# Performance work log

Hardware: AMD Instinct MI355X
Metric: run time of the kernel (lower is better)

The kernel has to match this reference:

```python
import jax, jax.numpy as jnp
import numpy as np

B, N, C, H = 8, 1024, 768, 12
HD = C // H  # 64


def setup_inputs() -> dict:
    key = jax.random.key(0)
    k0, k1, k2, k3, k4 = jax.random.split(key, 5)
    x = jax.random.normal(k0, (B, N, C), jnp.float32)
    # ToMe token sizes are counts >= 1; sample in [1, 16)
    size = jax.random.uniform(k1, (B, N, 1), jnp.float32, minval=1.0, maxval=16.0)
    key_padding_mask = jax.random.randint(k2, (B, N), 0, 2).astype(jnp.bool_)
    w_qkv = jax.random.normal(k3, (3 * C, C), jnp.float32) * (C ** -0.5)
    w_proj = jax.random.normal(k4, (C, C), jnp.float32) * (C ** -0.5)
    b_proj = jnp.zeros((C,), jnp.float32)
    return dict(x=x, size=size, key_padding_mask=key_padding_mask,
                w_qkv=w_qkv, w_proj=w_proj, b_proj=b_proj)


def reference(x, size, key_padding_mask, w_qkv, w_proj, b_proj):
    b, n, c = x.shape
    hd = c // H
    scale = hd ** -0.5
    # qkv projection: [B,N,3C] -> [3,B,H,N,hd]
    qkv = (x @ w_qkv.T).reshape(b, n, 3, H, hd).transpose(2, 0, 3, 1, 4)
    q, k, v = qkv[0], qkv[1], qkv[2]
    # raw scores [B,H,N,N]
    attn = jnp.einsum('bhnd,bhmd->bhnm', q, k) * scale
    # proportional attention: additive log-size bias over keys
    attn = attn + jnp.log(size)[:, None, None, :, 0]
    # key padding mask: True -> -inf
    attn = jnp.where(key_padding_mask[:, None, None, :], -jnp.inf, attn)
    attn = jax.nn.softmax(attn, axis=-1)
    # PV, back to [B,N,C]
    out = jnp.einsum('bhnm,bhmd->bnhd', attn, v).reshape(b, n, c)
    out = out @ w_proj.T + b_proj
    # mean of k over heads: [B,N,hd]
    k_mean = k.mean(axis=1)
    return out, k_mean
```

## Files before the change

kernel.cpp:

```cpp
#include <hip/hip_runtime.h>

typedef __bf16 bf16;
typedef __bf16 bf16x4 __attribute__((ext_vector_type(4)));
typedef __bf16 bf16x8 __attribute__((ext_vector_type(8)));
typedef float f32x4 __attribute__((ext_vector_type(4)));

#define MFMA_16x16x32(a, b, c) __builtin_amdgcn_mfma_f32_16x16x32_bf16((a), (b), (c), 0, 0, 0)

#define B_ 8
#define N_ 1024
#define C_ 768
#define H_ 12
#define HD_ 64
#define KDIM 768

__device__ __forceinline__ void gload_lds16(const void* g, void* l) {
  __builtin_amdgcn_global_load_lds(
      (const __attribute__((address_space(1))) void*)g,
      (__attribute__((address_space(3))) void*)l, 16, 0, 0);
}

__global__ __launch_bounds__(256) void detect_mask_kernel(const unsigned* __restrict__ m32,
                                                          int* __restrict__ flags) {
  const int i = blockIdx.x * 256 + threadIdx.x;
  if (i < 2048) {
    const unsigned v = m32[i];
    if (v > 1u) atomicOr(&flags[0], 1);
    if ((i & 1) && v != 0u) atomicOr(&flags[1], 1);
  }
}

__global__ __launch_bounds__(256) void cvt_kernel(const float* __restrict__ x,
                                                  const float* __restrict__ wq,
                                                  const float* __restrict__ wp,
                                                  const float* __restrict__ size_in,
                                                  const void* __restrict__ mask_raw,
                                                  const int* __restrict__ flags,
                                                  bf16* __restrict__ xb,
                                                  bf16* __restrict__ wqb,
                                                  bf16* __restrict__ wpb,
                                                  float* __restrict__ biasb) {
  const int i = blockIdx.x * 256 + threadIdx.x;
  {
    const float4 v = ((const float4*)x)[i];
    bf16x4 o = {(bf16)v.x, (bf16)v.y, (bf16)v.z, (bf16)v.w};
    ((bf16x4*)xb)[i] = o;
  }
  if (i < 442368) {
    const float4 v = ((const float4*)wq)[i];
    bf16x4 o = {(bf16)v.x, (bf16)v.y, (bf16)v.z, (bf16)v.w};
    ((bf16x4*)wqb)[i] = o;
  }
  if (i < 147456) {
    const float4 v = ((const float4*)wp)[i];
    bf16x4 o = {(bf16)v.x, (bf16)v.y, (bf16)v.z, (bf16)v.w};
    ((bf16x4*)wpb)[i] = o;
  }
  if (i < B_ * N_) {
    int mv;
    if (flags[0]) {
      mv = (int)((const unsigned char*)mask_raw)[i];
    } else if (flags[1]) {
      mv = ((const int*)mask_raw)[i];
    } else {
      const unsigned* m32 = (const unsigned*)mask_raw;
      mv = (int)(m32[2 * i] | m32[2 * i + 1]);
    }
    biasb[i] = mv ? -1e30f : logf(size_in[i]);
  }
}

template <int MODE>
__global__ __launch_bounds__(256) void gemm_bt(const bf16* __restrict__ A,
                                               const bf16* __restrict__ W,
                                               const float* __restrict__ bias,
                                               bf16* __restrict__ out0,
                                               bf16* __restrict__ out1,
                                               bf16* __restrict__ out2,
                                               float* __restrict__ outf) {
  __shared__ bf16 As[2][128 * 64];
  __shared__ bf16 Bs[2][128 * 64];
  const int bid = blockIdx.x;
  const int mt = bid % 64;
  const int nt = bid / 64;
  const int t = threadIdx.x;
  const int lane = t & 63, w = t >> 6;
  const int wm = w >> 1, wn = w & 1;
  const int l15 = lane & 15, lg = lane >> 4;

  f32x4 acc[4][4] = {};

  const int srow = t >> 3;
  const int skel = ((t & 7) ^ (srow & 7)) * 8;
  const bf16* Ag = A + (size_t)(mt * 128) * KDIM;
  const bf16* Bg = W + (size_t)(nt * 128) * KDIM;
  const int bA = mt >> 3;
  const int nbase = (mt & 7) * 128;

#define ASRC(st, c)                                                          \
  ((MODE == 0)                                                               \
       ? (Ag + (size_t)((c) * 32 + srow) * KDIM + (st) * 64 + skel)          \
       : (A + (((size_t)(bA * 12 + (st)) * 1024) + nbase + (c) * 32 + srow)  \
              * 64 + skel))
#define BSRC(st, c) (Bg + (size_t)((c) * 32 + srow) * KDIM + (st) * 64 + skel)

#pragma unroll
  for (int c = 0; c < 4; ++c) {
    gload_lds16(ASRC(0, c), (char*)As[0] + c * 4096 + w * 1024);
    gload_lds16(BSRC(0, c), (char*)Bs[0] + c * 4096 + w * 1024);
  }
  __syncthreads();

  const int swz = l15 & 7;

  for (int st = 0; st < KDIM / 64; ++st) {
    const int cur = st & 1;
    if (st < KDIM / 64 - 1) {
#pragma unroll
      for (int c = 0; c < 4; ++c) {
        gload_lds16(ASRC(st + 1, c), (char*)As[cur ^ 1] + c * 4096 + w * 1024);
        gload_lds16(BSRC(st + 1, c), (char*)Bs[cur ^ 1] + c * 4096 + w * 1024);
      }
    }
#pragma unroll
    for (int ks = 0; ks < 2; ++ks) {
      bf16x8 af[4], bfr[4];
#pragma unroll
      for (int i = 0; i < 4; ++i)
        af[i] = *(const bf16x8*)(As[cur] + (wm * 64 + i * 16 + l15) * 64 +
                                 ((ks * 4 + lg) ^ swz) * 8);
#pragma unroll
      for (int i = 0; i < 4; ++i)
        bfr[i] = *(const bf16x8*)(Bs[cur] + (wn * 64 + i * 16 + l15) * 64 +
                                  ((ks * 4 + lg) ^ swz) * 8);
#pragma unroll
      for (int i = 0; i < 4; ++i)
#pragma unroll
        for (int j = 0; j < 4; ++j)
          acc[i][j] = MFMA_16x16x32(af[i], bfr[j], acc[i][j]);
    }
    __syncthreads();
  }
#undef ASRC
#undef BSRC

  if (MODE == 0) {
    const int which = (nt * 128) / 768;
#pragma unroll
    for (int i = 0; i < 4; ++i)
#pragma unroll
      for (int j = 0; j < 4; ++j)
#pragma unroll
        for (int r = 0; r < 4; ++r) {
          const int m = mt * 128 + wm * 64 + i * 16 + lg * 4 + r;
          const int o = nt * 128 + wn * 64 + j * 16 + l15;
          const int b = m >> 10, n = m & 1023;
          const int f = o - which * 768;
          const int h = f >> 6, hd = f & 63;
          const bf16 bv = (bf16)acc[i][j][r];
          if (which == 0)
            out0[(((size_t)(b * 12 + h)) * 1024 + n) * 64 + hd] = bv;
          else if (which == 1)
            out1[(((size_t)(b * 12 + h)) * 1024 + n) * 64 + hd] = bv;
          else
            out2[(((size_t)(b * 12 + h)) * 64 + hd) * 1024 + n] = bv;
        }
  } else {
#pragma unroll
    for (int i = 0; i < 4; ++i)
#pragma unroll
      for (int j = 0; j < 4; ++j) {
        const int o = nt * 128 + wn * 64 + j * 16 + l15;
        const float bv = bias[o];
#pragma unroll
        for (int r = 0; r < 4; ++r) {
          const int m = mt * 128 + wm * 64 + i * 16 + lg * 4 + r;
          outf[(size_t)m * 768 + o] = acc[i][j][r] + bv;
        }
      }
  }
}

__global__ __launch_bounds__(256) void kmean_kernel(const bf16* __restrict__ kbuf,
                                                    float* __restrict__ kmean) {
  const int i = blockIdx.x * 256 + threadIdx.x;
  if (i >= B_ * N_ * HD_) return;
  const int hd = i & 63;
  const int n = (i >> 6) & 1023;
  const int b = i >> 16;
  float s = 0.f;
#pragma unroll
  for (int h = 0; h < 12; ++h)
    s += (float)kbuf[(((size_t)(b * 12 + h)) * 1024 + n) * 64 + hd];
  kmean[i] = s * (1.0f / 12.0f);
}

__global__ __launch_bounds__(512, 4) void attn_mfma(const bf16* __restrict__ qbuf,
                                                    const bf16* __restrict__ kbuf,
                                                    const bf16* __restrict__ vtbuf,
                                                    const float* __restrict__ biasb,
                                                    bf16* __restrict__ outws) {
  __shared__ bf16 Ks[2][4096];
  __shared__ bf16 Vs[2][4096];
  const int id = blockIdx.x;
  const int qt = id & 3;
  const int bh = id >> 2;
  const int b = bh / 12;
  const int t = threadIdx.x, lane = t & 63, w = t >> 6;
  const int l15 = lane & 15, lg = lane >> 4;
  const int qbase = qt * 256 + w * 16;

  const bf16* Q = qbuf + ((size_t)bh * 1024 + qbase) * 64;
  const bf16* Kp = kbuf + (size_t)bh * 65536;
  const bf16* Vt = vtbuf + (size_t)bh * 65536;
  const float* bias = biasb + b * 1024;

  const bf16x8 qb0 = *(const bf16x8*)(Q + l15 * 64 + lg * 8);
  const bf16x8 qb1 = *(const bf16x8*)(Q + l15 * 64 + 32 + lg * 8);
  const bf16x8 qc0 = *(const bf16x8*)(Q + (128 + l15) * 64 + lg * 8);
  const bf16x8 qc1 = *(const bf16x8*)(Q + (128 + l15) * 64 + 32 + lg * 8);

  const int srow = t >> 3;
  const int dsl = (t & 7) ^ (srow & 7);
  const int kkey = 32 * ((srow >> 5) & 1) + 4 * ((srow >> 4) & 1) +
                   8 * ((srow >> 2) & 3) + (srow & 3);
  const bf16* srcK = Kp + kkey * 64 + dsl * 8;
  const bf16* srcV = Vt + (size_t)srow * 1024 + dsl * 8;

  gload_lds16(srcK, (char*)&Ks[0][0] + w * 1024);
  gload_lds16(srcV, (char*)&Vs[0][0] + w * 1024);
  __syncthreads();

  const int bb0 = 8 * lg;
  const int swz = l15 & 7;

  f32x4 oacc[4] = {}, oacc2[4] = {};
  float m = -1e30f, l = 0.f;
  float m2 = -1e30f, l2 = 0.f;

  for (int kt = 0; kt < 16; ++kt) {
    const int cur = kt & 1;
    const int kb = kt * 64;
    if (kt < 15) {
      gload_lds16(srcK + (size_t)(kb + 64) * 64, (char*)&Ks[cur ^ 1][0] + w * 1024);
      gload_lds16(srcV + (kb + 64), (char*)&Vs[cur ^ 1][0] + w * 1024);
    }

    const bf16* LK = Ks[cur];
    const bf16* LV = Vs[cur];
    float sv[4][4], sw[4][4];
#pragma unroll
    for (int f = 0; f < 4; ++f) {
      const int cf = 32 * (f >> 1) + 4 * (f & 1);
      const bf16* kj = LK + (f * 16 + l15) * 64;
      const bf16x8 ka0 = *(const bf16x8*)(kj + (lg ^ swz) * 8);
      const bf16x8 ka1 = *(const bf16x8*)(kj + ((lg + 4) ^ swz) * 8);
      f32x4 z = {}, y = {};
      z = MFMA_16x16x32(ka0, qb0, z);
      y = MFMA_16x16x32(ka0, qc0, y);
      z = MFMA_16x16x32(ka1, qb1, z);
      y = MFMA_16x16x32(ka1, qc1, y);
      const float4 bi = *(const float4*)(bias + kb + cf + bb0);
      sv[f][0] = z[0] * 0.125f + bi.x;
      sv[f][1] = z[1] * 0.125f + bi.y;
      sv[f][2] = z[2] * 0.125f + bi.z;
      sv[f][3] = z[3] * 0.125f + bi.w;
      sw[f][0] = y[0] * 0.125f + bi.x;
      sw[f][1] = y[1] * 0.125f + bi.y;
      sw[f][2] = y[2] * 0.125f + bi.z;
      sw[f][3] = y[3] * 0.125f + bi.w;
    }
    float mx = sv[0][0], mx2 = sw[0][0];
#pragma unroll
    for (int f = 0; f < 4; ++f)
#pragma unroll
      for (int j = 0; j < 4; ++j) {
        mx = fmaxf(mx, sv[f][j]);
        mx2 = fmaxf(mx2, sw[f][j]);
      }
    mx = fmaxf(mx, __shfl_xor(mx, 16, 64));
    mx = fmaxf(mx, __shfl_xor(mx, 32, 64));
    mx2 = fmaxf(mx2, __shfl_xor(mx2, 16, 64));
    mx2 = fmaxf(mx2, __shfl_xor(mx2, 32, 64));
    const float mn = fmaxf(m, mx);
    const float mn2 = fmaxf(m2, mx2);
    const float resc = __expf(m - mn);
    const float resc2 = __expf(m2 - mn2);
    m = mn;
    m2 = mn2;

    float rs = 0.f, rs2 = 0.f;
    bf16x8 pa0, pa1, pa2, pa3;
#pragma unroll
    for (int f = 0; f < 4; ++f)
#pragma unroll
      for (int j = 0; j < 4; ++j) {
        const float p = __expf(sv[f][j] - mn);
        const float p2 = __expf(sw[f][j] - mn2);
        rs += p;
        rs2 += p2;
        const bf16 pb = (bf16)p;
        const bf16 pb2 = (bf16)p2;
        if (f == 0) { pa0[j] = pb; pa2[j] = pb2; }
        else if (f == 1) { pa0[4 + j] = pb; pa2[4 + j] = pb2; }
        else if (f == 2) { pa1[j] = pb; pa3[j] = pb2; }
        else { pa1[4 + j] = pb; pa3[4 + j] = pb2; }
      }
    rs += __shfl_xor(rs, 16, 64);
    rs += __shfl_xor(rs, 32, 64);
    rs2 += __shfl_xor(rs2, 16, 64);
    rs2 += __shfl_xor(rs2, 32, 64);
    l = l * resc + rs;
    l2 = l2 * resc2 + rs2;

#pragma unroll
    for (int df = 0; df < 4; ++df) {
      const bf16* vj = LV + (df * 16 + l15) * 64;
      const bf16x8 va0 = *(const bf16x8*)(vj + (lg ^ swz) * 8);
      const bf16x8 va1 = *(const bf16x8*)(vj + ((lg + 4) ^ swz) * 8);
      f32x4 t4 = oacc[df];
      f32x4 u4 = oacc2[df];
#pragma unroll
      for (int j = 0; j < 4; ++j) {
        t4[j] *= resc;
        u4[j] *= resc2;
      }
      t4 = MFMA_16x16x32(va0, pa0, t4);
      u4 = MFMA_16x16x32(va0, pa2, u4);
      t4 = MFMA_16x16x32(va1, pa1, t4);
      u4 = MFMA_16x16x32(va1, pa3, u4);
      oacc[df] = t4;
      oacc2[df] = u4;
    }
    __syncthreads();
  }

  const float inv = 1.0f / l;
  const float inv2 = 1.0f / l2;
  bf16* outp = outws + ((size_t)bh * 1024 + qbase + l15) * 64;
#pragma unroll
  for (int df = 0; df < 4; ++df) {
    bf16x4 ov = {(bf16)(oacc[df][0] * inv), (bf16)(oacc[df][1] * inv),
                 (bf16)(oacc[df][2] * inv), (bf16)(oacc[df][3] * inv)};
    *(bf16x4*)(outp + df * 16 + lg * 4) = ov;
    bf16x4 ov2 = {(bf16)(oacc2[df][0] * inv2), (bf16)(oacc2[df][1] * inv2),
                  (bf16)(oacc2[df][2] * inv2), (bf16)(oacc2[df][3] * inv2)};
    *(bf16x4*)(outp + (size_t)128 * 64 + df * 16 + lg * 4) = ov2;
  }
}

extern "C" void kernel_launch(void* const* d_in, const int* in_sizes, int n_in,
                              void* d_out, int out_size, void* d_ws, size_t ws_size,
                              hipStream_t stream) {
  const float* x       = (const float*)d_in[0];
  const float* size_in = (const float*)d_in[1];
  const void*  mask    = d_in[2];
  const float* w_qkv   = (const float*)d_in[3];
  const float* w_proj  = (const float*)d_in[4];
  const float* b_proj  = (const float*)d_in[5];
  float* out = (float*)d_out;

  if (n_in < 6 ||
      in_sizes[0] != 6291456 || in_sizes[1] != 8192 || in_sizes[2] != 8192 ||
      in_sizes[3] != 1769472 || in_sizes[4] != 589824 || in_sizes[5] != 768)
    return;

  const size_t QS = (size_t)B_ * H_ * N_ * HD_;
  if (ws_size < 55083024) return;

  bf16* xb    = (bf16*)d_ws;
  bf16* qbuf  = xb + QS;
  bf16* kbuf  = qbuf + QS;
  bf16* vtbuf = kbuf + QS;
  bf16* wqb   = vtbuf + QS;
  bf16* wpb   = wqb + 1769472;
  float* biasb = (float*)(wpb + 589824);
  int* flags = (int*)(biasb + 8192);
  bf16* attnw = xb;

  hipMemsetAsync(flags, 0, 8, stream);
  detect_mask_kernel<<<8, 256, 0, stream>>>((const unsigned*)mask, flags);
  cvt_kernel<<<6144, 256, 0, stream>>>(x, w_qkv, w_proj, size_in, mask, flags,
                                       xb, wqb, wpb, biasb);
  gemm_bt<0><<<64 * 18, 256, 0, stream>>>(xb, wqb, nullptr, qbuf, kbuf, vtbuf, nullptr);
  kmean_kernel<<<2048, 256, 0, stream>>>(kbuf, out + (size_t)B_ * N_ * C_);
  attn_mfma<<<384, 512, 0, stream>>>(qbuf, kbuf, vtbuf, biasb, attnw);
  gemm_bt<1><<<64 * 6, 256, 0, stream>>>(attnw, wpb, b_proj, nullptr, nullptr, nullptr, out);
}
```

Before: 165.5 us.

## Use 256x256 single-buffered tiles with 512 threads for QKV GEMM

Splits the templated GEMM into a dedicated QKV kernel and a projection kernel. The QKV GEMM moves from 128x128 tiles with 256 threads and double-buffered LDS to 256x256 tiles with 8 waves, each wave holding a 128x64 accumulator. The larger tile raises data reuse per LDS load and cuts the grid from 1152 to 288 blocks. In exchange it drops the double buffering, so loads and compute no longer overlap within a block. Register pressure also rises, and 288 blocks may leave some CUs on the 256-CU part underused.

```diff
diff --git a/kernel.cpp b/kernel.cpp
--- a/kernel.cpp
+++ b/kernel.cpp
@@ -70,14 +70,83 @@
   }
 }
 
-template <int MODE>
-__global__ __launch_bounds__(256) void gemm_bt(const bf16* __restrict__ A,
-                                               const bf16* __restrict__ W,
-                                               const float* __restrict__ bias,
-                                               bf16* __restrict__ out0,
-                                               bf16* __restrict__ out1,
-                                               bf16* __restrict__ out2,
-                                               float* __restrict__ outf) {
+__global__ __launch_bounds__(512, 2) void gemm_qkv(const bf16* __restrict__ A,
+                                                   const bf16* __restrict__ W,
+                                                   bf16* __restrict__ out0,
+                                                   bf16* __restrict__ out1,
+                                                   bf16* __restrict__ out2) {
+  __shared__ bf16 As[256 * 64];
+  __shared__ bf16 Bs[256 * 64];
+  const int bid = blockIdx.x;
+  const int mt = bid % 32;
+  const int nt = bid / 32;
+  const int t = threadIdx.x;
+  const int lane = t & 63, w = t >> 6;
+  const int wm = w >> 2, wn = w & 3;
+  const int l15 = lane & 15, lg = lane >> 4;
+
+  f32x4 acc[8][4] = {};
+
+  const int srow = t >> 3;
+  const int skel = ((t & 7) ^ (srow & 7)) * 8;
+  const bf16* Ag = A + (size_t)(mt * 256) * KDIM;
+  const bf16* Bg = W + (size_t)(nt * 256) * KDIM;
+
+  for (int st = 0; st < KDIM / 64; ++st) {
+    const int kt = st * 64;
+#pragma unroll
+    for (int c = 0; c < 4; ++c) {
+      gload_lds16(Ag + (size_t)(c * 64 + srow) * KDIM + kt + skel,
+                  (char*)As + c * 8192 + w * 1024);
+      gload_lds16(Bg + (size_t)(c * 64 + srow) * KDIM + kt + skel,
+                  (char*)Bs + c * 8192 + w * 1024);
+    }
+    __syncthreads();
+#pragma unroll
+    for (int ks = 0; ks < 2; ++ks) {
+      const int slot = ((ks * 4 + lg) ^ (l15 & 7)) * 8;
+      bf16x8 af[8], bfr[4];
+#pragma unroll
+      for (int i = 0; i < 8; ++i)
+        af[i] = *(const bf16x8*)(As + (wm * 128 + i * 16 + l15) * 64 + slot);
+#pragma unroll
+      for (int j = 0; j < 4; ++j)
+        bfr[j] = *(const bf16x8*)(Bs + (wn * 64 + j * 16 + l15) * 64 + slot);
+#pragma unroll
+      for (int i = 0; i < 8; ++i)
+#pragma unroll
+        for (int j = 0; j < 4; ++j)
+          acc[i][j] = MFMA_16x16x32(af[i], bfr[j], acc[i][j]);
+    }
+    __syncthreads();
+  }
+
+  const int which = nt / 3;
+#pragma unroll
+  for (int i = 0; i < 8; ++i)
+#pragma unroll
+    for (int j = 0; j < 4; ++j)
+#pragma unroll
+      for (int r = 0; r < 4; ++r) {
+        const int m = mt * 256 + wm * 128 + i * 16 + lg * 4 + r;
+        const int o = nt * 256 + wn * 64 + j * 16 + l15;
+        const int b = m >> 10, n = m & 1023;
+        const int f = o - which * 768;
+        const int h = f >> 6, hd = f & 63;
+        const bf16 bv = (bf16)acc[i][j][r];
+        if (which == 0)
+          out0[(((size_t)(b * 12 + h)) * 1024 + n) * 64 + hd] = bv;
+        else if (which == 1)
+          out1[(((size_t)(b * 12 + h)) * 1024 + n) * 64 + hd] = bv;
+        else
+          out2[(((size_t)(b * 12 + h)) * 64 + hd) * 1024 + n] = bv;
+      }
+}
+
+__global__ __launch_bounds__(256) void gemm_proj(const bf16* __restrict__ A,
+                                                 const bf16* __restrict__ W,
+                                                 const float* __restrict__ bias,
+                                                 float* __restrict__ outf) {
   __shared__ bf16 As[2][128 * 64];
   __shared__ bf16 Bs[2][128 * 64];
   const int bid = blockIdx.x;
@@ -92,16 +161,12 @@
 
   const int srow = t >> 3;
   const int skel = ((t & 7) ^ (srow & 7)) * 8;
-  const bf16* Ag = A + (size_t)(mt * 128) * KDIM;
   const bf16* Bg = W + (size_t)(nt * 128) * KDIM;
   const int bA = mt >> 3;
   const int nbase = (mt & 7) * 128;
 
 #define ASRC(st, c)                                                          \
-  ((MODE == 0)                                                               \
-       ? (Ag + (size_t)((c) * 32 + srow) * KDIM + (st) * 64 + skel)          \
-       : (A + (((size_t)(bA * 12 + (st)) * 1024) + nbase + (c) * 32 + srow)  \
-              * 64 + skel))
+  (A + (((size_t)(bA * 12 + (st)) * 1024) + nbase + (c) * 32 + srow) * 64 + skel)
 #define BSRC(st, c) (Bg + (size_t)((c) * 32 + srow) * KDIM + (st) * 64 + skel)
 
 #pragma unroll
@@ -144,41 +209,18 @@
 #undef ASRC
 #undef BSRC
 
-  if (MODE == 0) {
-    const int which = (nt * 128) / 768;
-#pragma unroll
-    for (int i = 0; i < 4; ++i)
-#pragma unroll
-      for (int j = 0; j < 4; ++j)
-#pragma unroll
-        for (int r = 0; r < 4; ++r) {
-          const int m = mt * 128 + wm * 64 + i * 16 + lg * 4 + r;
-          const int o = nt * 128 + wn * 64 + j * 16 + l15;
-          const int b = m >> 10, n = m & 1023;
-          const int f = o - which * 768;
-          const int h = f >> 6, hd = f & 63;
-          const bf16 bv = (bf16)acc[i][j][r];
-          if (which == 0)
-            out0[(((size_t)(b * 12 + h)) * 1024 + n) * 64 + hd] = bv;
-          else if (which == 1)
-            out1[(((size_t)(b * 12 + h)) * 1024 + n) * 64 + hd] = bv;
-          else
-            out2[(((size_t)(b * 12 + h)) * 64 + hd) * 1024 + n] = bv;
-        }
-  } else {
-#pragma unroll
-    for (int i = 0; i < 4; ++i)
-#pragma unroll
-      for (int j = 0; j < 4; ++j) {
-        const int o = nt * 128 + wn * 64 + j * 16 + l15;
-        const float bv = bias[o];
-#pragma unroll
-        for (int r = 0; r < 4; ++r) {
-          const int m = mt * 128 + wm * 64 + i * 16 + lg * 4 + r;
-          outf[(size_t)m * 768 + o] = acc[i][j][r] + bv;
-        }
-      }
-  }
+#pragma unroll
+  for (int i = 0; i < 4; ++i)
+#pragma unroll
+    for (int j = 0; j < 4; ++j) {
+      const int o = nt * 128 + wn * 64 + j * 16 + l15;
+      const float bv = bias[o];
+#pragma unroll
+      for (int r = 0; r < 4; ++r) {
+        const int m = mt * 128 + wm * 64 + i * 16 + lg * 4 + r;
+        outf[(size_t)m * 768 + o] = acc[i][j][r] + bv;
+      }
+    }
 }
 
 __global__ __launch_bounds__(256) void kmean_kernel(const bf16* __restrict__ kbuf,
@@ -382,8 +424,8 @@
   detect_mask_kernel<<<8, 256, 0, stream>>>((const unsigned*)mask, flags);
   cvt_kernel<<<6144, 256, 0, stream>>>(x, w_qkv, w_proj, size_in, mask, flags,
                                        xb, wqb, wpb, biasb);
-  gemm_bt<0><<<64 * 18, 256, 0, stream>>>(xb, wqb, nullptr, qbuf, kbuf, vtbuf, nullptr);
+  gemm_qkv<<<32 * 9, 512, 0, stream>>>(xb, wqb, qbuf, kbuf, vtbuf);
   kmean_kernel<<<2048, 256, 0, stream>>>(kbuf, out + (size_t)B_ * N_ * C_);
   attn_mfma<<<384, 512, 0, stream>>>(qbuf, kbuf, vtbuf, biasb, attnw);
-  gemm_bt<1><<<64 * 6, 256, 0, stream>>>(attnw, wpb, b_proj, nullptr, nullptr, nullptr, out);
-}
+  gemm_proj<<<64 * 6, 256, 0, stream>>>(attnw, wpb, b_proj, out);
+}
```

New measurement: 190.0 us. 14.8% more time.
